# Kernel optimization log

Measured on AMD Instinct MI355X. Metric: run time of the kernel, lower is better.

The kernel has to match this reference:

```python
import jax, jax.numpy as jnp
import numpy as np

NTOK, NINP, NREL = 50257, 512, 200
N, L, EPS = 1024, 64, 32  # n sequences, seq length, edges per sequence
E = N * EPS               # m.sum()


def setup_inputs() -> dict:
    key = jax.random.key(0)
    k1, k2, k3, k4 = jax.random.split(key, 4)
    seq = jax.random.randint(k1, (N, L), 0, NTOK, dtype=jnp.int32)
    m = jnp.full((N,), EPS, dtype=jnp.int32)          # edges per sequence (constant -> static E)
    rel = jax.random.randint(k2, (E,), 0, NREL, dtype=jnp.int32)
    emb = jax.random.normal(k3, (NTOK, NINP), dtype=jnp.float32)          # nn.Embedding weight
    W = 0.01 * jax.random.normal(k4, (NREL, NINP), dtype=jnp.float32)     # nn.Linear weight
    b = jnp.zeros((NREL,), dtype=jnp.float32)                             # nn.Linear bias
    return {"seq": seq, "m": m, "rel": rel, "emb": emb, "W": W, "b": b}


def reference(seq, m, rel, emb, W, b):
    # logit = linear(embedding(seq).sum(1))
    h = emb[seq].sum(axis=1)                    # (N, NINP) gather + segment-sum over tokens
    logit = h @ W.T + b                         # (N, NREL)

    # multi-label mask: mask[i, r] = True iff some edge of sequence i has relation r
    n_seq = m.shape[0]
    idx = jnp.repeat(jnp.arange(n_seq), m, total_repeat_length=rel.shape[0])  # (E,)
    mask = jnp.zeros((n_seq, logit.shape[1]), dtype=bool).at[idx, rel].set(True)

    # sum of logsigmoid on positive labels + log(1+1e-5 - sigmoid) on negatives, / len(seq)
    logp = jnp.sum(jnp.where(mask,
                             jax.nn.log_sigmoid(logit),
                             jnp.log(1.0 + 1e-5 - jax.nn.sigmoid(logit)))) / seq.shape[0]
    acc = jnp.mean(((logit > 0.5) == mask).astype(jnp.float32))
    return logp, acc
```

## Files before the change

kernel.cpp:

```cpp
#include <hip/hip_runtime.h>

#define NINP 512
#define NREL 200
#define LSEQ 64
#define WT_LD 256
#define SPB 4
#define NW 16

typedef float vfloat4 __attribute__((ext_vector_type(4)));

__global__ __launch_bounds__(256) void wt_kernel(
    const float* __restrict__ W,
    float* __restrict__ Wt,
    float* __restrict__ out)
{
    __shared__ float tile[64][65];
    const int b  = blockIdx.x;
    const int br = b >> 3, bk = b & 7;
    const int r0 = br * 64, k0 = bk * 64;
    const int t  = threadIdx.x;
    const int ty = t >> 6, tx = t & 63;

    if (b == 0 && t < 2) out[t] = 0.f;

    #pragma unroll
    for (int jj = 0; jj < 16; ++jj) {
        const int i = jj * 4 + ty;
        tile[i][tx] = (r0 + i < NREL) ? W[(r0 + i) * NINP + k0 + tx] : 0.f;
    }
    __syncthreads();
    #pragma unroll
    for (int jj = 0; jj < 16; ++jj) {
        const int k = k0 + jj * 4 + ty;
        Wt[k * WT_LD + r0 + tx] = tile[tx][jj * 4 + ty];
    }
}

__global__ __launch_bounds__(1024) void fused_kernel(
    const int* __restrict__ seq,
    const float* __restrict__ emb,
    const float* __restrict__ Wt,
    const int* __restrict__ rel,
    const float* __restrict__ bias,
    float* __restrict__ out,
    int N, int eps)
{
    __shared__ vfloat4 hpart[NW][2][64];
    __shared__ float4  h_pack4[NINP];
    __shared__ float4  pd[NW][SPB][64];
    __shared__ unsigned int maskbits[SPB][8];
    __shared__ float   red_lp[NW], red_ac[NW];

    const int i0   = blockIdx.x * SPB;
    const int t    = threadIdx.x;
    const int wave = __builtin_amdgcn_readfirstlane(t >> 6);
    const int lane = t & 63;

    if (t < SPB * 8) ((unsigned int*)maskbits)[t] = 0u;

    {
        const int sq = wave >> 2, qq = wave & 3;
        const int* sp = seq + (long)(i0 + sq) * LSEQ + qq * 16;
        vfloat4 lo = (vfloat4)0.f;
        vfloat4 hi = (vfloat4)0.f;
        #pragma unroll
        for (int j0 = 0; j0 < 16; j0 += 8) {
            const vfloat4* rp[8];
            #pragma unroll
            for (int j = 0; j < 8; ++j)
                rp[j] = (const vfloat4*)(emb +
                    (long)__builtin_amdgcn_readfirstlane(sp[j0 + j]) * NINP);
            vfloat4 l[8], h[8];
            #pragma unroll
            for (int j = 0; j < 8; ++j) {
                l[j] = __builtin_nontemporal_load(rp[j] + lane);
                h[j] = __builtin_nontemporal_load(rp[j] + 64 + lane);
            }
            #pragma unroll
            for (int j = 0; j < 4; ++j) {
                l[j] = l[2*j] + l[2*j+1];
                h[j] = h[2*j] + h[2*j+1];
            }
            lo += (l[0] + l[1]) + (l[2] + l[3]);
            hi += (h[0] + h[1]) + (h[2] + h[3]);
        }
        hpart[wave][0][lane] = lo;
        hpart[wave][1][lane] = hi;
    }
    __syncthreads();

    if (t < SPB * 32) {
        const int s = t >> 5, j = t & 31;
        if (j < eps) {
            int r = rel[(i0 + s) * eps + j];
            atomicOr(&maskbits[s][r >> 5], 1u << (r & 31));
        }
    }

    {
        const int kbase = wave * 32;
        const int p = lane >> 5;
        const int k = kbase + (lane & 31);
        const int fg = k >> 2, c = k & 3;
        const int half = fg >> 6, fl = fg & 63;
        float2 v;
        #pragma unroll
        for (int d = 0; d < 2; ++d) {
            const int sbar = 2 * p + d;
            float sum = 0.f;
            #pragma unroll
            for (int q = 0; q < 4; ++q)
                sum += ((const float*)&hpart[sbar * 4 + q][half][fl])[c];
            ((float*)&v)[d] = sum;
        }
        ((float2*)&h_pack4[k])[p] = v;
    }
    asm volatile("s_waitcnt lgkmcnt(0)" ::: "memory");
    __builtin_amdgcn_sched_barrier(0);

    {
        const float4* Wt4 = (const float4*)Wt;
        float4 a0 = make_float4(0.f, 0.f, 0.f, 0.f);
        float4 a1 = a0, a2 = a0, a3 = a0;
        const int kbase = wave * 32;
        #pragma unroll 4
        for (int k = kbase; k < kbase + 32; ++k) {
            const float4 wv = Wt4[k * 64 + lane];
            const float4 hp = h_pack4[k];
            a0.x += hp.x * wv.x; a0.y += hp.x * wv.y; a0.z += hp.x * wv.z; a0.w += hp.x * wv.w;
            a1.x += hp.y * wv.x; a1.y += hp.y * wv.y; a1.z += hp.y * wv.z; a1.w += hp.y * wv.w;
            a2.x += hp.z * wv.x; a2.y += hp.z * wv.y; a2.z += hp.z * wv.z; a2.w += hp.z * wv.w;
            a3.x += hp.w * wv.x; a3.y += hp.w * wv.y; a3.z += hp.w * wv.z; a3.w += hp.w * wv.w;
        }
        pd[wave][0][lane] = a0;
        pd[wave][1][lane] = a1;
        pd[wave][2][lane] = a2;
        pd[wave][3][lane] = a3;
    }
    __syncthreads();

    float term = 0.f, match = 0.f;
    {
        const int s = t >> 8;
        const int r = t & 255;
        if (r < NREL) {
            const int f = r >> 2, c = r & 3;
            float dot = bias[r];
            #pragma unroll
            for (int w = 0; w < NW; ++w)
                dot += ((const float*)&pd[w][s][f])[c];
            const unsigned mb = (maskbits[s][r >> 5] >> (r & 31)) & 1u;
            if (mb) {
                term = fminf(dot, 0.f) - log1pf(expf(-fabsf(dot)));
            } else {
                term = logf(1e-5f + 1.f / (1.f + expf(dot)));
            }
            match = (((dot > 0.5f) ? 1u : 0u) == mb) ? 1.f : 0.f;
        }
    }

    #pragma unroll
    for (int off = 32; off > 0; off >>= 1) {
        term  += __shfl_down(term,  off);
        match += __shfl_down(match, off);
    }
    if (lane == 0) { red_lp[wave] = term; red_ac[wave] = match; }
    __syncthreads();
    if (t == 0) {
        float s = 0.f, a = 0.f;
        #pragma unroll
        for (int w = 0; w < NW; ++w) { s += red_lp[w]; a += red_ac[w]; }
        atomicAdd(out + 0, s / (float)N);
        atomicAdd(out + 1, a / ((float)N * (float)NREL));
    }
}

extern "C" void kernel_launch(void* const* d_in, const int* in_sizes, int n_in,
                              void* d_out, int out_size, void* d_ws, size_t ws_size,
                              hipStream_t stream) {
    const int*   seq = (const int*)d_in[0];
    const int*   m   = (const int*)d_in[1]; (void)m;
    const int*   rel = (const int*)d_in[2];
    const float* emb = (const float*)d_in[3];
    const float* W   = (const float*)d_in[4];
    const float* b   = (const float*)d_in[5];
    float* out = (float*)d_out;

    const int N   = in_sizes[1];
    const int eps = in_sizes[2] / N;

    float* Wt = (float*)d_ws;

    wt_kernel<<<32, 256, 0, stream>>>(W, Wt, out);
    fused_kernel<<<N / SPB, 1024, 0, stream>>>(seq, emb, Wt, rel, b, out, N, eps);
}
```

Baseline: 172.1 us.

## Halve sequences per block to 2 with 512-thread blocks and move mask build earlier

```diff
diff --git a/kernel.cpp b/kernel.cpp
--- a/kernel.cpp
+++ b/kernel.cpp
@@ -4,8 +4,8 @@
 #define NREL 200
 #define LSEQ 64
 #define WT_LD 256
-#define SPB 4
-#define NW 16
+#define SPB 2
+#define NW 8
 
 typedef float vfloat4 __attribute__((ext_vector_type(4)));
 
@@ -36,7 +36,7 @@
     }
 }
 
-__global__ __launch_bounds__(1024) void fused_kernel(
+__global__ __launch_bounds__(512, 4) void fused_kernel(
     const int* __restrict__ seq,
     const float* __restrict__ emb,
     const float* __restrict__ Wt,
@@ -46,7 +46,7 @@
     int N, int eps)
 {
     __shared__ vfloat4 hpart[NW][2][64];
-    __shared__ float4  h_pack4[NINP];
+    __shared__ float2  h_pack2[NINP];
     __shared__ float4  pd[NW][SPB][64];
     __shared__ unsigned int maskbits[SPB][8];
     __shared__ float   red_lp[NW], red_ac[NW];
@@ -56,7 +56,14 @@
     const int wave = __builtin_amdgcn_readfirstlane(t >> 6);
     const int lane = t & 63;
 
-    if (t < SPB * 8) ((unsigned int*)maskbits)[t] = 0u;
+    if (wave == 0) {
+        if (lane < SPB * 8) ((unsigned int*)maskbits)[lane] = 0u;
+        const int s = lane >> 5, j = lane & 31;
+        if (j < eps) {
+            int r = rel[(i0 + s) * eps + j];
+            atomicOr(&maskbits[s][r >> 5], 1u << (r & 31));
+        }
+    }
 
     {
         const int sq = wave >> 2, qq = wave & 3;
@@ -89,31 +96,20 @@
     }
     __syncthreads();
 
-    if (t < SPB * 32) {
-        const int s = t >> 5, j = t & 31;
-        if (j < eps) {
-            int r = rel[(i0 + s) * eps + j];
-            atomicOr(&maskbits[s][r >> 5], 1u << (r & 31));
-        }
-    }
-
     {
-        const int kbase = wave * 32;
-        const int p = lane >> 5;
-        const int k = kbase + (lane & 31);
+        const int k = wave * 64 + lane;
         const int fg = k >> 2, c = k & 3;
         const int half = fg >> 6, fl = fg & 63;
         float2 v;
         #pragma unroll
-        for (int d = 0; d < 2; ++d) {
-            const int sbar = 2 * p + d;
+        for (int s = 0; s < SPB; ++s) {
             float sum = 0.f;
             #pragma unroll
             for (int q = 0; q < 4; ++q)
-                sum += ((const float*)&hpart[sbar * 4 + q][half][fl])[c];
-            ((float*)&v)[d] = sum;
+                sum += ((const float*)&hpart[s * 4 + q][half][fl])[c];
+            ((float*)&v)[s] = sum;
         }
-        ((float2*)&h_pack4[k])[p] = v;
+        h_pack2[k] = v;
     }
     asm volatile("s_waitcnt lgkmcnt(0)" ::: "memory");
     __builtin_amdgcn_sched_barrier(0);
@@ -121,21 +117,17 @@
     {
         const float4* Wt4 = (const float4*)Wt;
         float4 a0 = make_float4(0.f, 0.f, 0.f, 0.f);
-        float4 a1 = a0, a2 = a0, a3 = a0;
-        const int kbase = wave * 32;
+        float4 a1 = a0;
+        const int kbase = wave * 64;
         #pragma unroll 4
-        for (int k = kbase; k < kbase + 32; ++k) {
+        for (int k = kbase; k < kbase + 64; ++k) {
             const float4 wv = Wt4[k * 64 + lane];
-            const float4 hp = h_pack4[k];
+            const float2 hp = h_pack2[k];
             a0.x += hp.x * wv.x; a0.y += hp.x * wv.y; a0.z += hp.x * wv.z; a0.w += hp.x * wv.w;
             a1.x += hp.y * wv.x; a1.y += hp.y * wv.y; a1.z += hp.y * wv.z; a1.w += hp.y * wv.w;
-            a2.x += hp.z * wv.x; a2.y += hp.z * wv.y; a2.z += hp.z * wv.z; a2.w += hp.z * wv.w;
-            a3.x += hp.w * wv.x; a3.y += hp.w * wv.y; a3.z += hp.w * wv.z; a3.w += hp.w * wv.w;
         }
         pd[wave][0][lane] = a0;
         pd[wave][1][lane] = a1;
-        pd[wave][2][lane] = a2;
-        pd[wave][3][lane] = a3;
     }
     __syncthreads();
 
@@ -192,5 +184,5 @@
     float* Wt = (float*)d_ws;
 
     wt_kernel<<<32, 256, 0, stream>>>(W, Wt, out);
-    fused_kernel<<<N / SPB, 1024, 0, stream>>>(seq, emb, Wt, rel, b, out, N, eps);
+    fused_kernel<<<N / SPB, 512, 0, stream>>>(seq, emb, Wt, rel, b, out, N, eps);
 }
```

Result: slower. 191.4 us (+11.2%).
